# Performance work log

Hardware: AMD Instinct MI355X
Metric: run time of the kernel (lower is better)

## Reference

```python
import jax, jax.numpy as jnp
import numpy as np

OFFSET = 3  # windows 3,5,7


def _maxpool_same(x, k):
    # MaxPool2d(kernel=k, stride=1, padding=(k-1)//2); torch pads with -inf
    p = (k - 1) // 2
    return jax.lax.reduce_window(
        x, -jnp.inf, jax.lax.max,
        window_dimensions=(1, 1, k, k),
        window_strides=(1, 1, 1, 1),
        padding=((0, 0), (0, 0), (p, p), (p, p)))


def setup_inputs() -> dict:
    key = jax.random.key(0)
    # strictly positive so log10 is finite
    x = jax.random.uniform(key, (8, 64, 256, 256), dtype=jnp.float32,
                           minval=1e-3, maxval=1.0)
    return {"x": x}


def reference(x) -> jnp.ndarray:
    B, C, H, W = x.shape
    windows = jnp.array([2.0 * i + 1.0 for i in range(1, OFFSET + 1)],
                        dtype=x.dtype)  # [3,5,7]
    xs = jnp.log10(windows / (H * W))
    xc = xs - xs.mean()
    # Closed-form OLS slope weights: inv(X X^T) X reduces analytically to
    # w_i = (x_i - xbar) / sum_j (x_j - xbar)^2 for the slope row.
    w = xc / jnp.sum(xc * xc)                  # [OFFSET]
    # slope = sum_i w_i * log10(maxpool_{k_i}(x)), computed without stacking
    holder = jnp.zeros_like(x)
    for i in range(OFFSET):
        k = 2 * (i + 1) + 1
        holder = holder + w[i] * jnp.log10(_maxpool_same(x, k))
    return holder  # (B, C, H, W)
```

## Files before the change

kernel.cpp:

```cpp
#include <hip/hip_runtime.h>
#include <cmath>


#define IMG_H 256
#define IMG_W 256
#define RPW   8
#define NR    14
#define WPB   4

typedef float vf4 __attribute__((ext_vector_type(4)));

__device__ __forceinline__ vf4 aload(const float* base, uint32_t voff) {
  vf4 r;
  asm volatile("global_load_dwordx4 %0, %1, %2"
               : "=v"(r) : "v"(voff), "s"(base) : "memory");
  return r;
}

__device__ __forceinline__ void wait_first10(vf4& a, vf4& b, vf4& c, vf4& d,
                                             vf4& e, vf4& f, vf4& g, vf4& h,
                                             vf4& i, vf4& j) {
  asm volatile("s_waitcnt vmcnt(4)"
               : "+v"(a), "+v"(b), "+v"(c), "+v"(d), "+v"(e),
                 "+v"(f), "+v"(g), "+v"(h), "+v"(i), "+v"(j) :: "memory");
}

__device__ __forceinline__ void wait_last4(vf4& a, vf4& b, vf4& c, vf4& d) {
  asm volatile("s_waitcnt vmcnt(4)"
               : "+v"(a), "+v"(b), "+v"(c), "+v"(d) :: "memory");
}

__device__ __forceinline__ float dpp_left(float v) {
  return __int_as_float(
      __builtin_amdgcn_update_dpp(0, __float_as_int(v), 0x138, 0xF, 0xF, true));
}
__device__ __forceinline__ float dpp_right(float v) {
  return __int_as_float(
      __builtin_amdgcn_update_dpp(0, __float_as_int(v), 0x130, 0xF, 0xF, true));
}

__device__ __forceinline__ vf4 vmax(vf4 a, vf4 b) {
  vf4 r;
  r.x = fmaxf(a.x, b.x); r.y = fmaxf(a.y, b.y);
  r.z = fmaxf(a.z, b.z); r.w = fmaxf(a.w, b.w);
  return r;
}

struct PS { float p1, p2, p3, s1, s2, s3, f; };

__device__ __forceinline__ PS make_ps(vf4 a) {
  PS r;
  r.p1 = a.x;
  r.p2 = fmaxf(a.x, a.y);
  r.p3 = fmaxf(r.p2, a.z);
  r.s1 = a.w;
  r.s2 = fmaxf(a.z, a.w);
  r.s3 = fmaxf(a.y, r.s2);
  r.f  = fmaxf(r.p2, r.s2);
  return r;
}

__device__ __forceinline__ vf4 row_out(vf4 wm3, vf4 wm2, vf4 wm1, vf4 wc,
                                       vf4 wp1, vf4 wp2, vf4 wp3,
                                       float w3, float w5, float w7) {
  vf4 v1 = vmax(vmax(wm1, wc), wp1);
  vf4 v2 = vmax(v1, vmax(wm2, wp2));
  vf4 v3 = vmax(v2, vmax(wm3, wp3));

  PS a1 = make_ps(v1), a2 = make_ps(v2), a3 = make_ps(v3);

  float L1s1 = dpp_left(a1.s1);
  float L2s1 = dpp_left(a2.s1);
  float L2s2 = dpp_left(a2.s2);
  float L3s1 = dpp_left(a3.s1);
  float L3s2 = dpp_left(a3.s2);
  float L3s3 = dpp_left(a3.s3);

  float R1p1 = dpp_right(a1.p1);
  float R2p1 = dpp_right(a2.p1);
  float R2p2 = dpp_right(a2.p2);
  float R3p1 = dpp_right(a3.p1);
  float R3p2 = dpp_right(a3.p2);
  float R3p3 = dpp_right(a3.p3);

  float m3_0 = fmaxf(L1s1, a1.p2);
  float m3_1 = a1.p3;
  float m3_2 = a1.s3;
  float m3_3 = fmaxf(a1.s2, R1p1);

  float m5_0 = fmaxf(L2s2, a2.p3);
  float m5_1 = fmaxf(L2s1, a2.f);
  float m5_2 = fmaxf(a2.f, R2p1);
  float m5_3 = fmaxf(a2.s3, R2p2);

  float m7_0 = fmaxf(L3s3, a3.f);
  float m7_1 = fmaxf(fmaxf(L3s2, a3.f), R3p1);
  float m7_2 = fmaxf(fmaxf(L3s1, a3.f), R3p2);
  float m7_3 = fmaxf(a3.f, R3p3);

  vf4 o;
  o.x = fmaf(w7, __log2f(m7_0), fmaf(w5, __log2f(m5_0), w3 * __log2f(m3_0)));
  o.y = fmaf(w7, __log2f(m7_1), fmaf(w5, __log2f(m5_1), w3 * __log2f(m3_1)));
  o.z = fmaf(w7, __log2f(m7_2), fmaf(w5, __log2f(m5_2), w3 * __log2f(m3_2)));
  o.w = fmaf(w7, __log2f(m7_3), fmaf(w5, __log2f(m5_3), w3 * __log2f(m3_3)));
  return o;
}

__global__ __launch_bounds__(256, 6) void holder_kernel(
    const float* __restrict__ x, float* __restrict__ out,
    float w3, float w5, float w7)
{
  const int lane = threadIdx.x & 63;
  const int wave = threadIdx.x >> 6;
  const int img  = blockIdx.y;

  const int strip = ((blockIdx.x * WPB + wave) + img * 5) & 31;
  const int r0    = strip * RPW;

  const float* px = x + (size_t)img * (IMG_H * IMG_W);
  float*       po = out + (size_t)img * (IMG_H * IMG_W) + lane * 4;
  const uint32_t lo = (uint32_t)lane * 16u;

  const vf4 vzero = (vf4)0.0f;

  vf4 w[NR];
#pragma unroll
  for (int i = 0; i < NR; ++i) {
    int rr = r0 - 3 + i;
    int rc = rr < 0 ? 0 : (rr > IMG_H - 1 ? IMG_H - 1 : rr);
    w[i] = aload(px, (uint32_t)(rc * IMG_W * 4) + lo);
  }

  wait_first10(w[0], w[1], w[2], w[3], w[4], w[5], w[6], w[7], w[8], w[9]);
#pragma unroll
  for (int i = 0; i < 10; ++i) {
    if (r0 - 3 + i < 0) w[i] = vzero;
  }

#pragma unroll
  for (int j = 0; j < 4; ++j) {
    vf4 o = row_out(w[j], w[j + 1], w[j + 2], w[j + 3],
                    w[j + 4], w[j + 5], w[j + 6], w3, w5, w7);
    *(vf4*)(po + (r0 + j) * IMG_W) = o;
  }

  wait_last4(w[10], w[11], w[12], w[13]);
#pragma unroll
  for (int i = 10; i < NR; ++i) {
    if (r0 - 3 + i >= IMG_H) w[i] = vzero;
  }

#pragma unroll
  for (int j = 4; j < 8; ++j) {
    vf4 o = row_out(w[j], w[j + 1], w[j + 2], w[j + 3],
                    w[j + 4], w[j + 5], w[j + 6], w3, w5, w7);
    *(vf4*)(po + (r0 + j) * IMG_W) = o;
  }
}

extern "C" void kernel_launch(void* const* d_in, const int* in_sizes, int n_in,
                              void* d_out, int out_size, void* d_ws, size_t ws_size,
                              hipStream_t stream) {
  const float* x = (const float*)d_in[0];
  float* out = (float*)d_out;

  const int n_img = in_sizes[0] / (IMG_H * IMG_W);

  const double l0 = log10(3.0), l1 = log10(5.0), l2 = log10(7.0);
  const double m  = (l0 + l1 + l2) / 3.0;
  const double c0 = l0 - m, c1 = l1 - m, c2 = l2 - m;
  const double s  = c0 * c0 + c1 * c1 + c2 * c2;
  const double LG2 = 0.30102999566398119521;
  const float w3 = (float)(c0 / s * LG2);
  const float w5 = (float)(c1 / s * LG2);
  const float w7 = (float)(c2 / s * LG2);

  hipLaunchKernelGGL(holder_kernel, dim3(IMG_H / (WPB * RPW), n_img), dim3(256),
                     0, stream, x, out, w3, w5, w7);
}
```

Baseline: 233.1 us.

## Stream 32-row strips per wave with double-buffered prefetch of halo rows

Each single-wave block now handles a 32-row strip instead of an 8-row one. It slides a 14-row register window and prefetches the next 4 rows into alternating buffers while computing the current 4 output rows. This cuts the redundant halo loads (6 extra rows per 8 outputs becomes 6 per 32) and overlaps load latency with compute. In exchange it uses more registers, has fewer waves in flight, and depends on hand-counted vmcnt waits that interleave with stores.

```diff
diff --git a/kernel.cpp b/kernel.cpp
--- a/kernel.cpp
+++ b/kernel.cpp
@@ -4,9 +4,7 @@
 
 #define IMG_H 256
 #define IMG_W 256
-#define RPW   8
-#define NR    14
-#define WPB   4
+#define RPW   32
 
 typedef float vf4 __attribute__((ext_vector_type(4)));
 
@@ -17,16 +15,28 @@
   return r;
 }
 
-__device__ __forceinline__ void wait_first10(vf4& a, vf4& b, vf4& c, vf4& d,
-                                             vf4& e, vf4& f, vf4& g, vf4& h,
-                                             vf4& i, vf4& j) {
-  asm volatile("s_waitcnt vmcnt(4)"
+__device__ __forceinline__ void wait_pro(vf4& a, vf4& b, vf4& c, vf4& d,
+                                         vf4& e, vf4& f, vf4& g, vf4& h,
+                                         vf4& i, vf4& j) {
+  asm volatile("s_waitcnt vmcnt(8)"
                : "+v"(a), "+v"(b), "+v"(c), "+v"(d), "+v"(e),
                  "+v"(f), "+v"(g), "+v"(h), "+v"(i), "+v"(j) :: "memory");
 }
 
-__device__ __forceinline__ void wait_last4(vf4& a, vf4& b, vf4& c, vf4& d) {
-  asm volatile("s_waitcnt vmcnt(4)"
+__device__ __forceinline__ void wait_c0(vf4& a, vf4& b, vf4& c, vf4& d,
+                                        vf4& e, vf4& f, vf4& g, vf4& h) {
+  asm volatile("s_waitcnt vmcnt(8)"
+               : "+v"(a), "+v"(b), "+v"(c), "+v"(d),
+                 "+v"(e), "+v"(f), "+v"(g), "+v"(h) :: "memory");
+}
+
+__device__ __forceinline__ void wait_st(vf4& a, vf4& b, vf4& c, vf4& d) {
+  asm volatile("s_waitcnt vmcnt(12)"
+               : "+v"(a), "+v"(b), "+v"(c), "+v"(d) :: "memory");
+}
+
+__device__ __forceinline__ void wait_c5(vf4& a, vf4& b, vf4& c, vf4& d) {
+  asm volatile("s_waitcnt vmcnt(8)"
                : "+v"(a), "+v"(b), "+v"(c), "+v"(d) :: "memory");
 }
 
@@ -106,15 +116,13 @@
   return o;
 }
 
-__global__ __launch_bounds__(256, 6) void holder_kernel(
+__global__ __launch_bounds__(64, 4) void holder_kernel(
     const float* __restrict__ x, float* __restrict__ out,
     float w3, float w5, float w7)
 {
-  const int lane = threadIdx.x & 63;
-  const int wave = threadIdx.x >> 6;
-  const int img  = blockIdx.y;
-
-  const int strip = ((blockIdx.x * WPB + wave) + img * 5) & 31;
+  const int lane  = threadIdx.x;
+  const int img   = blockIdx.x;
+  const int strip = blockIdx.y;
   const int r0    = strip * RPW;
 
   const float* px = x + (size_t)img * (IMG_H * IMG_W);
@@ -123,38 +131,74 @@
 
   const vf4 vzero = (vf4)0.0f;
 
-  vf4 w[NR];
-#pragma unroll
-  for (int i = 0; i < NR; ++i) {
+  vf4 w[14], pa[4], pb[4];
+
+#pragma unroll
+  for (int i = 0; i < 14; ++i) {
     int rr = r0 - 3 + i;
-    int rc = rr < 0 ? 0 : (rr > IMG_H - 1 ? IMG_H - 1 : rr);
+    int rc = rr < 0 ? 0 : rr;
     w[i] = aload(px, (uint32_t)(rc * IMG_W * 4) + lo);
   }
-
-  wait_first10(w[0], w[1], w[2], w[3], w[4], w[5], w[6], w[7], w[8], w[9]);
-#pragma unroll
-  for (int i = 0; i < 10; ++i) {
-    if (r0 - 3 + i < 0) w[i] = vzero;
-  }
-
-#pragma unroll
-  for (int j = 0; j < 4; ++j) {
-    vf4 o = row_out(w[j], w[j + 1], w[j + 2], w[j + 3],
-                    w[j + 4], w[j + 5], w[j + 6], w3, w5, w7);
-    *(vf4*)(po + (r0 + j) * IMG_W) = o;
-  }
-
-  wait_last4(w[10], w[11], w[12], w[13]);
-#pragma unroll
-  for (int i = 10; i < NR; ++i) {
-    if (r0 - 3 + i >= IMG_H) w[i] = vzero;
-  }
-
-#pragma unroll
-  for (int j = 4; j < 8; ++j) {
-    vf4 o = row_out(w[j], w[j + 1], w[j + 2], w[j + 3],
-                    w[j + 4], w[j + 5], w[j + 6], w3, w5, w7);
-    *(vf4*)(po + (r0 + j) * IMG_W) = o;
+#pragma unroll
+  for (int j = 0; j < 4; ++j)
+    pa[j] = aload(px, (uint32_t)((r0 + 11 + j) * IMG_W * 4) + lo);
+
+  wait_pro(w[0], w[1], w[2], w[3], w[4], w[5], w[6], w[7], w[8], w[9]);
+  if (r0 == 0) { w[0] = vzero; w[1] = vzero; w[2] = vzero; }
+
+#pragma unroll
+  for (int c = 0; c < 8; ++c) {
+    if (c < 5) {
+      const int base = r0 + 15 + 4 * c;
+#pragma unroll
+      for (int j = 0; j < 4; ++j) {
+        int rr = base + j;
+        int rc = rr > IMG_H - 1 ? IMG_H - 1 : rr;
+        if (c & 1) pa[j] = aload(px, (uint32_t)(rc * IMG_W * 4) + lo);
+        else       pb[j] = aload(px, (uint32_t)(rc * IMG_W * 4) + lo);
+      }
+    }
+
+#pragma unroll
+    for (int j = 0; j < 4; ++j) {
+      vf4 o = row_out(w[j], w[j + 1], w[j + 2], w[j + 3],
+                      w[j + 4], w[j + 5], w[j + 6], w3, w5, w7);
+      *(vf4*)(po + (r0 + 4 * c + j) * IMG_W) = o;
+    }
+
+    if (c == 0) {
+      wait_c0(w[10], w[11], w[12], w[13], pa[0], pa[1], pa[2], pa[3]);
+#pragma unroll
+      for (int i = 0; i < 10; ++i) w[i] = w[i + 4];
+#pragma unroll
+      for (int j = 0; j < 4; ++j) w[10 + j] = pa[j];
+    } else if (c >= 1 && c <= 4) {
+      if (c & 1) {
+        wait_st(pb[0], pb[1], pb[2], pb[3]);
+#pragma unroll
+        for (int i = 0; i < 10; ++i) w[i] = w[i + 4];
+#pragma unroll
+        for (int j = 0; j < 4; ++j) w[10 + j] = pb[j];
+      } else {
+        wait_st(pa[0], pa[1], pa[2], pa[3]);
+#pragma unroll
+        for (int i = 0; i < 10; ++i) w[i] = w[i + 4];
+#pragma unroll
+        for (int j = 0; j < 4; ++j) w[10 + j] = pa[j];
+      }
+    } else if (c == 5) {
+      wait_c5(pb[0], pb[1], pb[2], pb[3]);
+#pragma unroll
+      for (int j = 0; j < 4; ++j)
+        if (r0 + 31 + j > IMG_H - 1) pb[j] = vzero;
+#pragma unroll
+      for (int i = 0; i < 10; ++i) w[i] = w[i + 4];
+#pragma unroll
+      for (int j = 0; j < 4; ++j) w[10 + j] = pb[j];
+    } else if (c == 6) {
+#pragma unroll
+      for (int i = 0; i < 10; ++i) w[i] = w[i + 4];
+    }
   }
 }
 
@@ -175,6 +219,6 @@
   const float w5 = (float)(c1 / s * LG2);
   const float w7 = (float)(c2 / s * LG2);
 
-  hipLaunchKernelGGL(holder_kernel, dim3(IMG_H / (WPB * RPW), n_img), dim3(256),
+  hipLaunchKernelGGL(holder_kernel, dim3(n_img, IMG_H / RPW), dim3(64),
                      0, stream, x, out, w3, w5, w7);
 }
```

New measurement: 235.1 us. About the same (+0.9%).
